# Performance work log

Measured on AMD Instinct MI355X. Metric: run time of the kernel, lower is better.

The kernel has to match this reference:

```python
import jax, jax.numpy as jnp
import numpy as np

NB, CIN, COUT, MID, G, K = 16, 128, 256, 128, 8, 64
GP = MID // G  # group_planes = 16
EPS = 1e-5


def _bn(x, g, b, axes):
    # train-mode batchnorm (biased var), channel axis = 1
    m = jnp.mean(x, axes, keepdims=True)
    v = jnp.var(x, axes, keepdims=True)
    sh = (1, -1) + (1,) * (x.ndim - 2)
    return g.reshape(sh) * (x - m) * jax.lax.rsqrt(v + EPS) + b.reshape(sh)


def _axial(x, qkv_w, bq_g, bq_b, bs_g, bs_b, bo_g, bo_b, rel):
    # x: [B, MID, K]; attention along last axis
    B = x.shape[0]
    qkv = _bn(jnp.einsum('oc,bcl->bol', qkv_w, x), bq_g, bq_b, (0, 2))
    qkv = qkv.reshape(B, G, 2 * GP, K)
    q, k, v = qkv[:, :, :GP // 2], qkv[:, :, GP // 2:GP], qkv[:, :, GP:]
    # relative position embedding lookup: rel [2*GP, 2K-1]
    idx = jnp.arange(K)[:, None] - jnp.arange(K)[None, :] + K - 1  # [K,K]
    emb = rel[:, idx]  # [2*GP, K, K]
    q_e, k_e, v_e = emb[:GP // 2], emb[GP // 2:GP], emb[GP:]
    qr = 0.1 * jnp.einsum('bgci,cij->bgij', q, q_e)          # f_qr = 0.1
    kr = 0.1 * jnp.einsum('bgci,cij->bgji', k, k_e)          # f_kr, transpose fused
    qk = jnp.einsum('bgci,bgcj->bgij', q, k)
    sim = jnp.concatenate([qk, qr, kr], axis=1)              # [B, 3G, K, K]
    sim = _bn(sim, bs_g, bs_b, (0, 2, 3)).reshape(B, 3, G, K, K).sum(1)
    sim = jax.nn.softmax(sim, axis=-1)                       # [B, G, K, K]
    sv = jnp.einsum('bgij,bgcj->bgci', sim, v)               # f_sv = 1.0
    sve = 0.1 * jnp.einsum('bgij,cij->bgci', sim, v_e)       # f_sve = 0.1
    out = jnp.concatenate([sv, sve], axis=1).reshape(B, 2 * MID, K)
    out = _bn(out, bo_g, bo_b, (0, 2))
    return out.reshape(B, MID, 2, K).sum(2)                  # [B, MID, K]


def _block(x, c1_w, c1_b, cd_w, cd_b, bn1_g, bn1_b,
           h_qkv_w, h_bq_g, h_bq_b, h_bs_g, h_bs_b, h_bo_g, h_bo_b, h_rel,
           w_qkv_w, w_bq_g, w_bq_b, w_bs_g, w_bs_b, w_bo_g, w_bo_b, w_rel,
           cu_w, cu_b, bn2_g, bn2_b):
    x_out = jnp.einsum('oc,nchw->nohw', c1_w, x) + c1_b[None, :, None, None]
    out = jnp.einsum('oc,nchw->nohw', cd_w, x) + cd_b[None, :, None, None]
    out = jax.nn.relu(_bn(out, bn1_g, bn1_b, (0, 2, 3)))
    N = out.shape[0]
    # height block: x.permute(0,3,1,2) -> [N, W, C, H] -> [N*W, C, H]
    h_in = out.transpose(0, 3, 1, 2).reshape(N * K, MID, K)
    h = _axial(h_in, h_qkv_w, h_bq_g, h_bq_b, h_bs_g, h_bs_b, h_bo_g, h_bo_b, h_rel)
    h = h.reshape(N, K, MID, K).transpose(0, 2, 3, 1)  # [N, C, H, W]
    # width block: x.permute(0,2,1,3) -> [N, H, C, W] -> [N*H, C, W]
    w_in = h.transpose(0, 2, 1, 3).reshape(N * K, MID, K)
    w = _axial(w_in, w_qkv_w, w_bq_g, w_bq_b, w_bs_g, w_bs_b, w_bo_g, w_bo_b, w_rel)
    w = w.reshape(N, K, MID, K).transpose(0, 2, 1, 3)  # [N, C, H, W]
    out = jnp.einsum('oc,nchw->nohw', cu_w, w) + cu_b[None, :, None, None]
    out = _bn(out, bn2_g, bn2_b, (0, 2, 3))
    return out + x_out


def setup_inputs() -> dict:
    key = jax.random.key(0)
    ks = jax.random.split(key, 12)
    d = {}
    d['x'] = jax.random.normal(ks[0], (NB, CIN, K, K), jnp.float32)
    d['c1_w'] = jax.random.normal(ks[1], (COUT, CIN), jnp.float32) * np.sqrt(1.0 / CIN)
    d['c1_b'] = jnp.zeros((COUT,), jnp.float32)
    d['cd_w'] = jax.random.normal(ks[2], (MID, CIN), jnp.float32) * np.sqrt(1.0 / CIN)
    d['cd_b'] = jnp.zeros((MID,), jnp.float32)
    d['bn1_g'] = jnp.ones((MID,), jnp.float32); d['bn1_b'] = jnp.zeros((MID,), jnp.float32)
    for i, p in enumerate(['h_', 'w_']):
        d[p + 'qkv_w'] = jax.random.normal(ks[3 + i], (2 * MID, MID), jnp.float32) * np.sqrt(1.0 / MID)
        d[p + 'bq_g'] = jnp.ones((2 * MID,), jnp.float32); d[p + 'bq_b'] = jnp.zeros((2 * MID,), jnp.float32)
        d[p + 'bs_g'] = jnp.ones((3 * G,), jnp.float32); d[p + 'bs_b'] = jnp.zeros((3 * G,), jnp.float32)
        d[p + 'bo_g'] = jnp.ones((2 * MID,), jnp.float32); d[p + 'bo_b'] = jnp.zeros((2 * MID,), jnp.float32)
        d[p + 'rel'] = jax.random.normal(ks[5 + i], (2 * GP, 2 * K - 1), jnp.float32) * np.sqrt(1.0 / GP)
    d['cu_w'] = jax.random.normal(ks[7], (COUT, MID), jnp.float32) * np.sqrt(1.0 / MID)
    d['cu_b'] = jnp.zeros((COUT,), jnp.float32)
    d['bn2_g'] = jnp.ones((COUT,), jnp.float32); d['bn2_b'] = jnp.zeros((COUT,), jnp.float32)
    return d


def reference(x, c1_w, c1_b, cd_w, cd_b, bn1_g, bn1_b,
              h_qkv_w, h_bq_g, h_bq_b, h_bs_g, h_bs_b, h_bo_g, h_bo_b, h_rel,
              w_qkv_w, w_bq_g, w_bq_b, w_bs_g, w_bs_b, w_bo_g, w_bo_b, w_rel,
              cu_w, cu_b, bn2_g, bn2_b):
    return _block(x, c1_w, c1_b, cd_w, cd_b, bn1_g, bn1_b,
                  h_qkv_w, h_bq_g, h_bq_b, h_bs_g, h_bs_b, h_bo_g, h_bo_b, h_rel,
                  w_qkv_w, w_bq_g, w_bq_b, w_bs_g, w_bs_b, w_bo_g, w_bo_b, w_rel,
                  cu_w, cu_b, bn2_g, bn2_b)
```

## Files before the change

### kernel.cpp

```cpp
#include <hip/hip_runtime.h>


#define NCOPY 64

typedef __attribute__((ext_vector_type(8))) short bf16x8;
typedef __attribute__((ext_vector_type(4))) short bf16x4;
typedef __attribute__((ext_vector_type(4))) float f32x4;
typedef __attribute__((ext_vector_type(2))) float f32x2;

__device__ __forceinline__ float wave_sum(float v){
  #pragma unroll
  for (int o = 32; o; o >>= 1) v += __shfl_xor(v, o, 64);
  return v;
}
__device__ __forceinline__ ushort f2bf(float f){
  union { float f; unsigned u; } v; v.f = f;
  unsigned r = v.u + 0x7FFFu + ((v.u >> 16) & 1u);
  return (ushort)(r >> 16);
}
__device__ __forceinline__ float bf2f(ushort u){
  union { unsigned u; float f; } v; v.u = ((unsigned)u) << 16;
  return v.f;
}

__global__ void k_cvt5(const float* __restrict__ s0, const float* __restrict__ s1,
                       const float* __restrict__ s2, const float* __restrict__ s3,
                       const float* __restrict__ s4, ushort* __restrict__ dst){
  int i = blockIdx.x*256 + threadIdx.x;
  if (i >= 147456) return;
  float v;
  if      (i < 16384)  v = s0[i];
  else if (i < 49152)  v = s1[i-16384];
  else if (i < 81920)  v = s2[i-49152];
  else if (i < 114688) v = s3[i-81920];
  else                 v = s4[i-114688];
  dst[i] = f2bf(v);
}

template<int O, int MODE, int SLOG, int INBF, int OUTBF>
__global__ __launch_bounds__(256) void k_gemm(
    const void* __restrict__ X_, const ushort* __restrict__ Wb,
    const float* __restrict__ bias, void* __restrict__ out_,
    float* __restrict__ acc, const ushort* __restrict__ y2,
    const float* __restrict__ scsh, ushort* __restrict__ vout)
{
  constexpr int RPW = O/4;
  constexpr int NS  = RPW/16;
  __shared__ ushort XT[64*128];

  const int tid = threadIdx.x;
  const int col0 = blockIdx.x << 6;
  const int seg  = col0 >> SLOG;
  const int p0   = col0 & ((1<<SLOG)-1);

  {
    const int col = tid & 63;
    const int kc8 = tid >> 6;
    #pragma unroll
    for (int q = 0; q < 4; ++q){
      int kc = kc8*4 + q;
      int c0 = kc*8;
      bf16x8 pk;
      if constexpr (INBF){
        const ushort* xb = (const ushort*)X_ + (((size_t)seg*128) << SLOG) + p0 + col;
        #pragma unroll
        for (int j = 0; j < 8; ++j)
          pk[j] = (short)xb[(size_t)(c0+j) << SLOG];
      } else {
        const float* xb = (const float*)X_ + (((size_t)seg*128) << SLOG) + p0 + col;
        #pragma unroll
        for (int j = 0; j < 8; ++j)
          pk[j] = (short)f2bf(xb[(size_t)(c0+j) << SLOG]);
      }
      *(bf16x8*)&XT[col*128 + ((kc ^ (col & 15)) << 3)] = pk;
    }
  }
  __syncthreads();

  const int lane = tid & 63;
  const int wid  = tid >> 6;
  const int l15  = lane & 15, lg = lane >> 4;

  f32x4 accr[NS][4];
  #pragma unroll
  for (int s = 0; s < NS; ++s)
    #pragma unroll
    for (int ns = 0; ns < 4; ++ns)
      accr[s][ns] = (f32x4){0.f,0.f,0.f,0.f};

  #pragma unroll
  for (int kk = 0; kk < 4; ++kk){
    bf16x8 af[NS];
    #pragma unroll
    for (int s = 0; s < NS; ++s){
      int m = wid*RPW + s*16 + l15;
      af[s] = *(const bf16x8*)(Wb + (size_t)m*128 + kk*32 + lg*8);
    }
    bf16x8 bfr[4];
    #pragma unroll
    for (int ns = 0; ns < 4; ++ns){
      int ncol  = ns*16 + l15;
      int chunk = kk*4 + lg;
      bfr[ns] = *(const bf16x8*)&XT[ncol*128 + ((chunk ^ l15) << 3)];
    }
    #pragma unroll
    for (int s = 0; s < NS; ++s)
      #pragma unroll
      for (int ns = 0; ns < 4; ++ns)
        accr[s][ns] = __builtin_amdgcn_mfma_f32_16x16x32_bf16(
                        af[s], bfr[ns], accr[s][ns], 0, 0, 0);
  }

  float* accb = (MODE != 2) ? acc + (size_t)(blockIdx.x & (NCOPY-1))*2*O : nullptr;
  #pragma unroll
  for (int s = 0; s < NS; ++s){
    #pragma unroll
    for (int r = 0; r < 4; ++r){
      const int m = wid*RPW + s*16 + lg*4 + r;
      const float bs = (MODE == 0 || MODE == 2) ? bias[m] : 0.f;
      float vsum = 0.f, vsq = 0.f;
      #pragma unroll
      for (int ns = 0; ns < 4; ++ns){
        float v = accr[s][ns][r] + bs;
        if constexpr (MODE == 3){
          const int cm = ((m >> 5) << 4) + (m & 15);
          size_t oidx = (((size_t)seg*128 + cm) << SLOG) + p0 + ns*16 + l15;
          if ((s & 1) == 0) ((float*)out_)[oidx] = v;
          else              vout[oidx] = f2bf(v);
        } else {
          size_t oidx = (((size_t)seg*O + m) << SLOG) + p0 + ns*16 + l15;
          if (MODE == 2)
            v += fmaf(scsh[m], bf2f(y2[oidx]), scsh[O+m]);
          if constexpr (OUTBF) ((ushort*)out_)[oidx] = f2bf(v);
          else                 ((float*) out_)[oidx] = v;
        }
        vsum += v; vsq = fmaf(v, v, vsq);
      }
      if (MODE != 2){
        #pragma unroll
        for (int o2 = 1; o2 < 16; o2 <<= 1){
          vsum += __shfl_xor(vsum, o2, 64);
          vsq  += __shfl_xor(vsq , o2, 64);
        }
        if (l15 == 0){
          atomicAdd(&accb[m],   vsum);
          atomicAdd(&accb[O+m], vsq);
        }
      }
    }
  }
}

__global__ void k_finalize(const float* __restrict__ acc, const float* __restrict__ g,
    const float* __restrict__ b, float* __restrict__ scsh, int C, float invcnt)
{
  int c = blockIdx.x*blockDim.x + threadIdx.x;
  if (c >= C) return;
  float s = 0.f, s2 = 0.f;
  #pragma unroll 4
  for (int k2 = 0; k2 < NCOPY; ++k2){
    s  += acc[(size_t)k2*2*C + c];
    s2 += acc[(size_t)k2*2*C + C + c];
  }
  float mean = s*invcnt;
  float var  = s2*invcnt - mean*mean;
  float sc = g[c]*rsqrtf(var + 1e-5f);
  scsh[c]   = sc;
  scsh[C+c] = fmaf(-mean, sc, b[c]);
}

__global__ __launch_bounds__(256) void k_trans_bnrelu(const ushort* __restrict__ out0,
    const float* __restrict__ scsh, ushort* __restrict__ hin)
{
  __shared__ float t[64][66];
  const int c = blockIdx.x, n = blockIdx.y;
  const int tid = threadIdx.x;
  const float sc = scsh[c], sh = scsh[128+c];
  const uint* src = (const uint*)(out0 + ((size_t)n*128 + c)*4096);
  #pragma unroll
  for (int r = 0; r < 8; ++r){
    int u = tid + r*256;
    uint a = src[u];
    f32x2 vv; vv.x = bf2f((ushort)a); vv.y = bf2f((ushort)(a >> 16));
    *(f32x2*)&t[u >> 5][(u & 31)*2] = vv;
  }
  __syncthreads();
  uint* dst = (uint*)(hin + (size_t)(n*64)*8192 + (size_t)c*64);
  #pragma unroll
  for (int r = 0; r < 8; ++r){
    int u = tid + r*256;
    int w = u >> 5, hp = u & 31;
    float v0 = fmaxf(fmaf(sc, t[2*hp    ][w], sh), 0.f);
    float v1 = fmaxf(fmaf(sc, t[2*hp + 1][w], sh), 0.f);
    dst[(size_t)w*4096 + hp] = ((uint)f2bf(v1) << 16) | f2bf(v0);
  }
}

__global__ __launch_bounds__(256) void k_prep_rel2(const float* __restrict__ relh,
    const float* __restrict__ relw, float* __restrict__ rwh, float* __restrict__ rww)
{
  const float* rel = (blockIdx.x & 2) ? relw : relh;
  float* rw        = (blockIdx.x & 2) ? rww  : rwh;
  const int side = blockIdx.x & 1;
  const float* base = rel + side*8*127;
  float* Wout = rw + side*4096;
  float* Sout = rw + 8192 + side*512;
  const int tid = threadIdx.y*64 + threadIdx.x;
  for (int idx = tid; idx < 4096; idx += 256){
    int pr = idx >> 6, i = idx & 63;
    int c = pr >> 3, c2 = pr & 7;
    const float* r1 = base + c*127 + i;
    const float* r2 = base + c2*127 + i;
    float s = 0.f;
    #pragma unroll 8
    for (int u = 0; u < 64; ++u) s = fmaf(r1[u], r2[u], s);
    Wout[idx] = s;
  }
  for (int idx = tid; idx < 512; idx += 256){
    int c = idx >> 6, i = idx & 63;
    const float* r1 = base + c*127 + i;
    float s = 0.f;
    #pragma unroll 8
    for (int u = 0; u < 64; ++u) s += r1[u];
    Sout[idx] = s;
  }
}

__global__ __launch_bounds__(256, 4) void k_att_stats(const float* __restrict__ qk32,
    const float* __restrict__ bq, const float* __restrict__ rw, float* __restrict__ accsim)
{
  __shared__ float WqS[4096], WkS[4096], SqS[512], SkS[512];
  const int b = blockIdx.x;
  const int tx = threadIdx.x, ty = threadIdx.y;
  const int tid = ty*64 + tx;
  for (int idx = tid; idx < 4096; idx += 256){ WqS[idx] = rw[idx]; WkS[idx] = rw[4096+idx]; }
  for (int idx = tid; idx < 512;  idx += 256){ SqS[idx] = rw[8192+idx]; SkS[idx] = rw[8704+idx]; }
  __syncthreads();
  float* accb = accsim + (size_t)(b & (NCOPY-1)) * 48;
  const int i = tx;
  const int l15 = tx & 15, lg = tx >> 4;
  const short one_bf = (short)0x3F80;
  const bf16x8 ones = {one_bf,one_bf,one_bf,one_bf,one_bf,one_bf,one_bf,one_bf};

  #pragma unroll
  for (int gi = 0; gi < 2; ++gi){
    const int g = ty*2 + gi;
    float q[8], k[8];
    #pragma unroll
    for (int c = 0; c < 8; ++c){
      int oq = g*32 + c, ok = oq + 8;
      q[c] = fmaf(bq[oq], qk32[((size_t)b*128 + g*16 + c    )*64 + i], bq[256+oq]);
      k[c] = fmaf(bq[ok], qk32[((size_t)b*128 + g*16 + 8 + c)*64 + i], bq[256+ok]);
    }
    const int och = g*32 + l15;
    const float gsc = bq[och], gsh = bq[256+och];
    const float* src = &qk32[((size_t)b*128 + g*16 + l15)*64 + lg*8];
    bf16x8 a0, a1;
    #pragma unroll
    for (int j = 0; j < 8; ++j) a0[j] = (short)f2bf(fmaf(gsc, src[j],      gsh));
    #pragma unroll
    for (int j = 0; j < 8; ++j) a1[j] = (short)f2bf(fmaf(gsc, src[32 + j], gsh));
    f32x4 G = (f32x4){0.f,0.f,0.f,0.f};
    f32x4 R = (f32x4){0.f,0.f,0.f,0.f};
    G = __builtin_amdgcn_mfma_f32_16x16x32_bf16(a0, a0, G, 0, 0, 0);
    G = __builtin_amdgcn_mfma_f32_16x16x32_bf16(a1, a1, G, 0, 0, 0);
    R = __builtin_amdgcn_mfma_f32_16x16x32_bf16(a0, ones, R, 0, 0, 0);
    R = __builtin_amdgcn_mfma_f32_16x16x32_bf16(a1, ones, R, 0, 0, 0);
    float ss = 0.f, sqk = 0.f;
    const bool gq_lane = (l15 < 8) && (lg < 2);
    const bool r_lane  = (l15 == 0) && (lg < 2);
    #pragma unroll
    for (int r = 0; r < 4; ++r){
      float gsw = __shfl_xor(G[r], 40, 64);
      float rsw = __shfl_xor(R[r], 32, 64);
      if (gq_lane) ss  = fmaf(G[r], gsw, ss);
      if (r_lane)  sqk = fmaf(R[r], rsw, sqk);
    }
    float aq = 0.f, ak = 0.f, aq2 = 0.f, ak2 = 0.f;
    #pragma unroll
    for (int c = 0; c < 8; ++c){
      aq = fmaf(q[c], SqS[c*64 + i], aq);
      ak = fmaf(k[c], SkS[c*64 + i], ak);
    }
    #pragma unroll
    for (int c = 0; c < 8; ++c){
      #pragma unroll
      for (int c2 = c; c2 < 8; ++c2){
        float w2 = (c2 == c) ? 1.f : 2.f;
        aq2 = fmaf(w2*q[c]*q[c2], WqS[(c*8+c2)*64 + i], aq2);
        ak2 = fmaf(w2*k[c]*k[c2], WkS[(c*8+c2)*64 + i], ak2);
      }
    }
    sqk = wave_sum(sqk);  ss  = wave_sum(ss);
    aq  = wave_sum(aq);   ak  = wave_sum(ak);
    aq2 = wave_sum(aq2);  ak2 = wave_sum(ak2);
    if (tx == 0){
      atomicAdd(&accb[g],      sqk);       atomicAdd(&accb[24+g],    ss);
      atomicAdd(&accb[8+g],    0.1f*aq);   atomicAdd(&accb[24+8+g],  0.01f*aq2);
      atomicAdd(&accb[16+g],   0.1f*ak);   atomicAdd(&accb[24+16+g], 0.01f*ak2);
    }
  }
}

__global__ __launch_bounds__(256) void k_att2(const float* __restrict__ qk32,
    const ushort* __restrict__ vbf, const float* __restrict__ bq,
    const float* __restrict__ rel, const float* __restrict__ simsc,
    ushort* __restrict__ svout, float* __restrict__ accbo)
{
  __shared__ __align__(16) char smem[32768];
  float* REQT = (float*)(smem);
  float* REKT = (float*)(smem + 6144);
  float* KT   = (float*)(smem + 12288);
  float* MP   = (float*)(smem + 30720);
  float* SP   = (float*)(smem + 31744);
  float* RINV = (float*)(smem + 30720);

  const int b = blockIdx.x, g = blockIdx.y;
  const int tx = threadIdx.x, ty = threadIdx.y;
  const int tid = ty*64 + tx;
  const float scq  = simsc[g];
  const float scr_ = 0.1f*simsc[8+g];
  const float sck_ = 0.1f*simsc[16+g];

  if (tid < 128){
    int j = tid & 63, h = tid >> 6;
    f32x4 kv;
    #pragma unroll
    for (int e = 0; e < 4; ++e){
      int o = g*32 + 8 + h*4 + e;
      kv[e] = fmaf(bq[o], qk32[((size_t)b*128 + g*16 + 8 + h*4 + e)*64 + j], bq[256+o]);
    }
    *(f32x4*)(KT + j*8 + h*4) = kv;
  }
  if (tid < 254){
    int side = tid >= 127;
    int d = tid - side*127;
    float rs = side ? sck_ : scr_;
    float* dst = (side ? REKT : REQT) + d*12;
    f32x4 r0, r1;
    #pragma unroll
    for (int e = 0; e < 4; ++e) r0[e] = rel[(side*8 + e)*127 + d]*rs;
    #pragma unroll
    for (int e = 0; e < 4; ++e) r1[e] = rel[(side*8 + 4 + e)*127 + d]*rs;
    *(f32x4*)dst = r0; *(f32x4*)(dst+4) = r1;
  }
  {
    int c = tid >> 4, j4 = (tid & 15)*4;
    int o = g*32 + 16 + c;
    float gsc = bq[o], gsh = bq[256+o];
    const ushort* src = &vbf[((size_t)b*128 + g*16 + c)*64 + j4];
    bf16x4 pv;
    #pragma unroll
    for (int e = 0; e < 4; ++e) pv[e] = (short)f2bf(fmaf(gsc, bf2f(src[e]), gsh));
    *(bf16x4*)(smem + 24576 + c*128 + (((j4>>3) ^ (c&7))<<4) + (j4&7)*2) = pv;
  }
  {
    int c = tid >> 4, d8 = (tid & 15)*8;
    const float* rsrc = &rel[(16+c)*127 + d8];
    bf16x8 pk;
    #pragma unroll
    for (int e = 0; e < 8; ++e){
      int d = d8 + e;
      pk[e] = (d < 127) ? (short)f2bf(0.1f*rsrc[e]) : (short)0;
    }
    *(bf16x8*)(smem + 26624 + c*256 + (((d8>>3) ^ (c&15))<<4)) = pk;
  }
  float q8[8], qs8[8];
  #pragma unroll
  for (int c = 0; c < 8; ++c){
    int o = g*32 + c;
    float qv = fmaf(bq[o], qk32[((size_t)b*128 + g*16 + c)*64 + tx], bq[256+o]);
    q8[c] = qv; qs8[c] = scq*qv;
  }
  __syncthreads();

  float acc[16];
  {
    const int j0 = ty*16;
    const f32x2* q2  = (const f32x2*)q8;
    const f32x2* qs2 = (const f32x2*)qs8;
    #pragma unroll
    for (int t = 0; t < 16; ++t){
      const int j = j0 + t;
      const f32x2* kt = (const f32x2*)(KT + j*8);
      const f32x2* rq = (const f32x2*)(REQT + (tx - j + 63)*12);
      const f32x2* rk = (const f32x2*)(REKT + (j - tx + 63)*12);
      f32x2 a2 = (f32x2){0.f, 0.f};
      #pragma unroll
      for (int c2 = 0; c2 < 4; ++c2){
        f32x2 ktv = kt[c2];
        a2 = __builtin_elementwise_fma(qs2[c2], ktv,    a2);
        a2 = __builtin_elementwise_fma(q2[c2],  rq[c2], a2);
        a2 = __builtin_elementwise_fma(ktv,     rk[c2], a2);
      }
      acc[t] = a2.x + a2.y;
    }
  }
  {
    float m0 = fmaxf(fmaxf(acc[0],acc[1]),  fmaxf(acc[2],acc[3]));
    float m1 = fmaxf(fmaxf(acc[4],acc[5]),  fmaxf(acc[6],acc[7]));
    float m2 = fmaxf(fmaxf(acc[8],acc[9]),  fmaxf(acc[10],acc[11]));
    float m3 = fmaxf(fmaxf(acc[12],acc[13]),fmaxf(acc[14],acc[15]));
    MP[ty*64 + tx] = fmaxf(fmaxf(m0,m1), fmaxf(m2,m3));
  }
  __syncthreads();

  {
    f32x4 z = (f32x4){0.f,0.f,0.f,0.f};
    float* zp = (float*)(smem + 8192 + tid*64);
    *(f32x4*)(zp+0) = z; *(f32x4*)(zp+4) = z;
    *(f32x4*)(zp+8) = z; *(f32x4*)(zp+12) = z;
  }
  {
    float mrow = fmaxf(fmaxf(MP[tx], MP[64+tx]), fmaxf(MP[128+tx], MP[192+tx]));
    float s = 0.f;
    #pragma unroll
    for (int t = 0; t < 16; ++t){ float ex = __expf(acc[t]-mrow); acc[t] = ex; s += ex; }
    SP[ty*64 + tx] = s;
  }
  __syncthreads();

  if (ty == 0)
    RINV[tx] = 1.0f / ((SP[tx] + SP[64+tx]) + (SP[128+tx] + SP[192+tx]));
  {
    bf16x8 pk0, pk1;
    #pragma unroll
    for (int e = 0; e < 8; ++e){ pk0[e] = (short)f2bf(acc[e]); pk1[e] = (short)f2bf(acc[8+e]); }
    char* pbbase = smem + 0 + tx*128;
    *(bf16x8*)(pbbase + (((2*ty    ) ^ (tx&7))<<4)) = pk0;
    *(bf16x8*)(pbbase + (((2*ty + 1) ^ (tx&7))<<4)) = pk1;
    char* ppbase = smem + 8192 + tx*256;
    #pragma unroll
    for (int e = 0; e < 16; ++e){
      int j = ty*16 + e, d = tx - j + 63;
      *(ushort*)(ppbase + (((d>>3) ^ (tx&15))<<4) + (d&7)*2) = f2bf(acc[e]);
    }
  }
  __syncthreads();

  {
    const int l15 = tx & 15, lg = tx >> 4;
    const int i0 = ty*16;
    const int rowA = i0 + l15;
    char* pbA = smem + 0    + rowA*128;
    char* ppA = smem + 8192 + rowA*256;
    char* vbB = smem + 24576 + l15*128;
    char* reB = smem + 26624 + l15*256;
    f32x4 accv = (f32x4){0.f,0.f,0.f,0.f};
    f32x4 acce = (f32x4){0.f,0.f,0.f,0.f};
    #pragma unroll
    for (int kk = 0; kk < 2; ++kk){
      bf16x8 a  = *(bf16x8*)(pbA + (((kk*4+lg) ^ (rowA&7))<<4));
      bf16x8 bb = *(bf16x8*)(vbB + (((kk*4+lg) ^ (l15&7))<<4));
      accv = __builtin_amdgcn_mfma_f32_16x16x32_bf16(a, bb, accv, 0, 0, 0);
    }
    #pragma unroll
    for (int kk = 0; kk < 4; ++kk){
      bf16x8 a  = *(bf16x8*)(ppA + (((kk*4+lg) ^ (rowA&15))<<4));
      bf16x8 bb = *(bf16x8*)(reB + (((kk*4+lg) ^ (l15&15))<<4));
      acce = __builtin_amdgcn_mfma_f32_16x16x32_bf16(a, bb, acce, 0, 0, 0);
    }
    f32x4 ri4 = *(f32x4*)(smem + 30720 + (i0 + lg*4)*4);
    float* accb = accbo + (size_t)(b & (NCOPY-1)) * 512;
    {
      bf16x4 vb4;
      float vsum = 0.f, vsq = 0.f;
      #pragma unroll
      for (int r = 0; r < 4; ++r){
        float v = accv[r]*ri4[r];
        vb4[r] = (short)f2bf(v); vsum += v; vsq = fmaf(v, v, vsq);
      }
      int ch = g*16 + l15;
      *(bf16x4*)&svout[((size_t)b*256 + ch)*64 + i0 + lg*4] = vb4;
      vsum += __shfl_xor(vsum, 16, 64); vsum += __shfl_xor(vsum, 32, 64);
      vsq  += __shfl_xor(vsq , 16, 64); vsq  += __shfl_xor(vsq , 32, 64);
      if (lg == 0){ atomicAdd(&accb[ch], vsum); atomicAdd(&accb[256+ch], vsq); }
    }
    {
      bf16x4 vb4;
      float vsum = 0.f, vsq = 0.f;
      #pragma unroll
      for (int r = 0; r < 4; ++r){
        float v = acce[r]*ri4[r];
        vb4[r] = (short)f2bf(v); vsum += v; vsq = fmaf(v, v, vsq);
      }
      int ch = 128 + g*16 + l15;
      *(bf16x4*)&svout[((size_t)b*256 + ch)*64 + i0 + lg*4] = vb4;
      vsum += __shfl_xor(vsum, 16, 64); vsum += __shfl_xor(vsum, 32, 64);
      vsq  += __shfl_xor(vsq , 16, 64); vsq  += __shfl_xor(vsq , 32, 64);
      if (lg == 0){ atomicAdd(&accb[ch], vsum); atomicAdd(&accb[256+ch], vsq); }
    }
  }
}

__global__ __launch_bounds__(256) void k_pairT(const ushort* __restrict__ sv,
    const float* __restrict__ bo, ushort* __restrict__ win)
{
  __shared__ float t[64][66];
  const int c = blockIdx.x, n = blockIdx.y;
  const int tid = threadIdx.x;
  const float s0 = bo[2*c], s1 = bo[2*c+1];
  const float sh = bo[256 + 2*c] + bo[256 + 2*c + 1];
  const ushort* base = sv + (size_t)(n*64)*256*64;
  #pragma unroll
  for (int r = 0; r < 8; ++r){
    int u = tid + r*256;
    int w = u >> 5, hp = u & 31;
    uint a = *(const uint*)&base[((size_t)w*256 + 2*c    )*64 + 2*hp];
    uint bwd = *(const uint*)&base[((size_t)w*256 + 2*c + 1)*64 + 2*hp];
    float a0 = bf2f((ushort)a),   a1 = bf2f((ushort)(a >> 16));
    float b0 = bf2f((ushort)bwd), b1 = bf2f((ushort)(bwd >> 16));
    f32x2 vv;
    vv.x = fmaf(s0, a0, fmaf(s1, b0, sh));
    vv.y = fmaf(s0, a1, fmaf(s1, b1, sh));
    *(f32x2*)&t[w][2*hp] = vv;
  }
  __syncthreads();
  uint* dst = (uint*)(win + (size_t)(n*64)*8192 + (size_t)c*64);
  #pragma unroll
  for (int r = 0; r < 8; ++r){
    int u = tid + r*256;
    int h = u >> 5, wp = u & 31;
    float v0 = t[2*wp    ][h];
    float v1 = t[2*wp + 1][h];
    dst[(size_t)h*4096 + wp] = ((uint)f2bf(v1) << 16) | f2bf(v0);
  }
}

__global__ __launch_bounds__(256) void k_pair_w(const ushort* __restrict__ sv,
    const float* __restrict__ bo, ushort* __restrict__ wbuf)
{
  const int m = blockIdx.x, n = blockIdx.y;
  const int tid = threadIdx.x;
  const float s0 = bo[2*m], s1 = bo[2*m+1];
  const float sh = bo[256 + 2*m] + bo[256 + 2*m + 1];
  const uint* p0 = (const uint*)(sv + ((size_t)(n*64)*256 + 2*m    )*64);
  const uint* p1 = (const uint*)(sv + ((size_t)(n*64)*256 + 2*m + 1)*64);
  uint* dst = (uint*)(wbuf + ((size_t)(n*128 + m)*64)*64);
  #pragma unroll
  for (int r = 0; r < 8; ++r){
    int u = tid + r*256;
    int h = u >> 5, wp = u & 31;
    uint a = p0[(size_t)h*8192 + wp];
    uint bwd = p1[(size_t)h*8192 + wp];
    float a0 = bf2f((ushort)a),   a1 = bf2f((ushort)(a >> 16));
    float b0 = bf2f((ushort)bwd), b1 = bf2f((ushort)(bwd >> 16));
    float r0 = fmaf(s0, a0, fmaf(s1, b0, sh));
    float r1 = fmaf(s0, a1, fmaf(s1, b1, sh));
    dst[(size_t)u] = ((uint)f2bf(r1) << 16) | f2bf(r0);
  }
}


extern "C" void kernel_launch(void* const* d_in, const int* in_sizes, int n_in,
                              void* d_out, int out_size, void* d_ws, size_t ws_size,
                              hipStream_t stream)
{
  const float* x     = (const float*)d_in[0];
  const float* c1_w  = (const float*)d_in[1];
  const float* c1_b  = (const float*)d_in[2];
  const float* cd_w  = (const float*)d_in[3];
  const float* cd_b  = (const float*)d_in[4];
  const float* bn1_g = (const float*)d_in[5];
  const float* bn1_b = (const float*)d_in[6];
  const float* h_qkv = (const float*)d_in[7];
  const float* h_bqg = (const float*)d_in[8];
  const float* h_bqb = (const float*)d_in[9];
  const float* h_bsg = (const float*)d_in[10];
  const float* h_bsb = (const float*)d_in[11];
  const float* h_bog = (const float*)d_in[12];
  const float* h_bob = (const float*)d_in[13];
  const float* h_rel = (const float*)d_in[14];
  const float* w_qkv = (const float*)d_in[15];
  const float* w_bqg = (const float*)d_in[16];
  const float* w_bqb = (const float*)d_in[17];
  const float* w_bsg = (const float*)d_in[18];
  const float* w_bsb = (const float*)d_in[19];
  const float* w_bog = (const float*)d_in[20];
  const float* w_bob = (const float*)d_in[21];
  const float* w_rel = (const float*)d_in[22];
  const float* cu_w  = (const float*)d_in[23];
  const float* cu_b  = (const float*)d_in[24];
  const float* bn2_g = (const float*)d_in[25];
  const float* bn2_b = (const float*)d_in[26];
  float* out = (float*)d_out;
  char* ws = (char*)d_ws;

  ushort* OUT0  = (ushort*)(ws + 0);
  ushort* HIN   = (ushort*)(ws + (32ull<<20));
  float*  QK32H = (float*)(ws + (64ull<<20));
  ushort* VBFH  = (ushort*)(ws + (96ull<<20));
  ushort* SVO   = (ushort*)(ws + 0);
  ushort* WIN   = (ushort*)(ws + (64ull<<20));
  float*  QK32W = (float*)(ws + (96ull<<20));
  ushort* VBFW  = (ushort*)(ws + (128ull<<20));
  ushort* WBUF  = (ushort*)(ws + (64ull<<20));
  ushort* Y2    = (ushort*)(ws + (96ull<<20));
  float*  ST    = (float*)(ws + (160ull<<20));

  float* ACC_BN1 = ST;
  float* ACC_BQ  = ST + 16384;
  float* ACC_SIM = ST + 49152;
  float* ACC_BO  = ST + 52224;
  float* ACC_BQW = ST + 84992;
  float* ACC_SIMW= ST + 117760;
  float* ACC_BOW = ST + 120832;
  float* ACC_BN2 = ST + 153600;
  float* SCB     = ST + 186368;
  float* SC_BN1 = SCB;        float* SC_BQ  = SCB + 256;
  float* SC_SIM = SCB + 768;  float* SC_BO  = SCB + 816;
  float* SC_BQW = SCB + 1328; float* SC_SIMW= SCB + 1840;
  float* SC_BOW = SCB + 1888; float* SC_BN2 = SCB + 2400;
  float* RWH  = ST + 189280;
  float* RWW  = ST + 198496;
  ushort* CDBF = (ushort*)(ST + 207712);
  ushort* QHBF = CDBF + 16384;
  ushort* QWBF = CDBF + 49152;
  ushort* CUBF = CDBF + 81920;
  ushort* C1BF = CDBF + 114688;

  hipMemsetAsync(ST, 0, 186368*sizeof(float), stream);

  const dim3 blk(64,4);
  const float inv64k = 1.f/65536.f;
  const float invsim = 1.f/4194304.f;

  k_cvt5<<<576, 256, 0, stream>>>(cd_w, h_qkv, w_qkv, cu_w, c1_w, CDBF);
  k_prep_rel2<<<4, blk, 0, stream>>>(h_rel, w_rel, RWH, RWW);

  k_gemm<128,0,12,0,1><<<1024, 256, 0, stream>>>(x, CDBF, cd_b, OUT0, ACC_BN1, nullptr, nullptr, nullptr);
  k_finalize<<<1, 128, 0, stream>>>(ACC_BN1, bn1_g, bn1_b, SC_BN1, 128, inv64k);
  k_trans_bnrelu<<<dim3(128,16), 256, 0, stream>>>(OUT0, SC_BN1, HIN);

  k_gemm<256,3,6,1,0><<<1024, 256, 0, stream>>>(HIN, QHBF, nullptr, QK32H, ACC_BQ, nullptr, nullptr, VBFH);
  k_finalize<<<1, 256, 0, stream>>>(ACC_BQ, h_bqg, h_bqb, SC_BQ, 256, inv64k);
  k_att_stats<<<1024, blk, 0, stream>>>(QK32H, SC_BQ, RWH, ACC_SIM);
  k_finalize<<<1, 32, 0, stream>>>(ACC_SIM, h_bsg, h_bsb, SC_SIM, 24, invsim);
  k_att2<<<dim3(1024,8), blk, 0, stream>>>(QK32H, VBFH, SC_BQ, h_rel, SC_SIM, SVO, ACC_BO);
  k_finalize<<<1, 256, 0, stream>>>(ACC_BO, h_bog, h_bob, SC_BO, 256, inv64k);
  k_pairT<<<dim3(128,16), 256, 0, stream>>>(SVO, SC_BO, WIN);

  k_gemm<256,3,6,1,0><<<1024, 256, 0, stream>>>(WIN, QWBF, nullptr, QK32W, ACC_BQW, nullptr, nullptr, VBFW);
  k_finalize<<<1, 256, 0, stream>>>(ACC_BQW, w_bqg, w_bqb, SC_BQW, 256, inv64k);
  k_att_stats<<<1024, blk, 0, stream>>>(QK32W, SC_BQW, RWW, ACC_SIMW);
  k_finalize<<<1, 32, 0, stream>>>(ACC_SIMW, w_bsg, w_bsb, SC_SIMW, 24, invsim);
  k_att2<<<dim3(1024,8), blk, 0, stream>>>(QK32W, VBFW, SC_BQW, w_rel, SC_SIMW, SVO, ACC_BOW);
  k_finalize<<<1, 256, 0, stream>>>(ACC_BOW, w_bog, w_bob, SC_BOW, 256, inv64k);
  k_pair_w<<<dim3(128,16), 256, 0, stream>>>(SVO, SC_BOW, WBUF);

  k_gemm<256,0,12,1,1><<<1024, 256, 0, stream>>>(WBUF, CUBF, cu_b, Y2, ACC_BN2, nullptr, nullptr, nullptr);
  k_finalize<<<1, 256, 0, stream>>>(ACC_BN2, bn2_g, bn2_b, SC_BN2, 256, inv64k);
  k_gemm<256,2,12,0,0><<<1024, 256, 0, stream>>>(x, C1BF, c1_b, out, nullptr, Y2, SC_BN2, nullptr);
}
```

Baseline: 375.6 us.

## Merge prep kernels, store triangular rel-pair table, pair two rows in att2 logits

Fuses the weight-conversion and relative-embedding prep kernels into one launch. The pairwise rel product table now holds only the upper-triangular 36 channel pairs instead of 64, which shrinks the att_stats shared-memory footprint so the launch bound can rise from 4 to 7 blocks per CU. The att2 logit loop now handles two key positions per iteration, loading KT with wider vector reads and keeping separate accumulators. The aim is fewer launches, higher occupancy and more instruction-level parallelism, in exchange for extra register pressure and some index arithmetic.

```diff
diff --git a/kernel.cpp b/kernel.cpp
--- a/kernel.cpp
+++ b/kernel.cpp
@@ -23,18 +23,53 @@
   return v.f;
 }
 
-__global__ void k_cvt5(const float* __restrict__ s0, const float* __restrict__ s1,
-                       const float* __restrict__ s2, const float* __restrict__ s3,
-                       const float* __restrict__ s4, ushort* __restrict__ dst){
-  int i = blockIdx.x*256 + threadIdx.x;
-  if (i >= 147456) return;
-  float v;
-  if      (i < 16384)  v = s0[i];
-  else if (i < 49152)  v = s1[i-16384];
-  else if (i < 81920)  v = s2[i-49152];
-  else if (i < 114688) v = s3[i-81920];
-  else                 v = s4[i-114688];
-  dst[i] = f2bf(v);
+__global__ void k_pre(const float* __restrict__ s0, const float* __restrict__ s1,
+                      const float* __restrict__ s2, const float* __restrict__ s3,
+                      const float* __restrict__ s4, ushort* __restrict__ dst,
+                      const float* __restrict__ relh, const float* __restrict__ relw,
+                      float* __restrict__ rwh, float* __restrict__ rww){
+  const int blk = blockIdx.x;
+  if (blk < 576){
+    int i = blk*256 + threadIdx.x;
+    if (i >= 147456) return;
+    float v;
+    if      (i < 16384)  v = s0[i];
+    else if (i < 49152)  v = s1[i-16384];
+    else if (i < 81920)  v = s2[i-49152];
+    else if (i < 114688) v = s3[i-81920];
+    else                 v = s4[i-114688];
+    dst[i] = f2bf(v);
+  } else {
+    const int sidx = blk - 576;
+    const float* rel = (sidx & 2) ? relw : relh;
+    float* rw        = (sidx & 2) ? rww  : rwh;
+    const int side = sidx & 1;
+    const float* base = rel + side*8*127;
+    float* Wout = rw + side*2304;
+    float* Sout = rw + 4608 + side*512;
+    const int tid = threadIdx.x;
+    for (int idx = tid; idx < 2304; idx += 256){
+      int pr = idx >> 6, i = idx & 63;
+      int c = 0, off = pr;
+      #pragma unroll
+      for (int cc = 0; cc < 7; ++cc){ if (off >= 8 - c){ off -= (8 - c); ++c; } }
+      int c2 = c + off;
+      const float* r1 = base + c*127 + i;
+      const float* r2 = base + c2*127 + i;
+      float s = 0.f;
+      #pragma unroll 8
+      for (int u = 0; u < 64; ++u) s = fmaf(r1[u], r2[u], s);
+      Wout[idx] = s;
+    }
+    for (int idx = tid; idx < 512; idx += 256){
+      int c = idx >> 6, i = idx & 63;
+      const float* r1 = base + c*127 + i;
+      float s = 0.f;
+      #pragma unroll 8
+      for (int u = 0; u < 64; ++u) s += r1[u];
+      Sout[idx] = s;
+    }
+  }
 }
 
 template<int O, int MODE, int SLOG, int INBF, int OUTBF>
@@ -196,51 +231,22 @@
   }
 }
 
-__global__ __launch_bounds__(256) void k_prep_rel2(const float* __restrict__ relh,
-    const float* __restrict__ relw, float* __restrict__ rwh, float* __restrict__ rww)
-{
-  const float* rel = (blockIdx.x & 2) ? relw : relh;
-  float* rw        = (blockIdx.x & 2) ? rww  : rwh;
-  const int side = blockIdx.x & 1;
-  const float* base = rel + side*8*127;
-  float* Wout = rw + side*4096;
-  float* Sout = rw + 8192 + side*512;
-  const int tid = threadIdx.y*64 + threadIdx.x;
-  for (int idx = tid; idx < 4096; idx += 256){
-    int pr = idx >> 6, i = idx & 63;
-    int c = pr >> 3, c2 = pr & 7;
-    const float* r1 = base + c*127 + i;
-    const float* r2 = base + c2*127 + i;
-    float s = 0.f;
-    #pragma unroll 8
-    for (int u = 0; u < 64; ++u) s = fmaf(r1[u], r2[u], s);
-    Wout[idx] = s;
-  }
-  for (int idx = tid; idx < 512; idx += 256){
-    int c = idx >> 6, i = idx & 63;
-    const float* r1 = base + c*127 + i;
-    float s = 0.f;
-    #pragma unroll 8
-    for (int u = 0; u < 64; ++u) s += r1[u];
-    Sout[idx] = s;
-  }
-}
-
-__global__ __launch_bounds__(256, 4) void k_att_stats(const float* __restrict__ qk32,
+__global__ __launch_bounds__(256, 7) void k_att_stats(const float* __restrict__ qk32,
     const float* __restrict__ bq, const float* __restrict__ rw, float* __restrict__ accsim)
 {
-  __shared__ float WqS[4096], WkS[4096], SqS[512], SkS[512];
+  __shared__ float WqS[2304], WkS[2304], SqS[512], SkS[512];
   const int b = blockIdx.x;
   const int tx = threadIdx.x, ty = threadIdx.y;
   const int tid = ty*64 + tx;
-  for (int idx = tid; idx < 4096; idx += 256){ WqS[idx] = rw[idx]; WkS[idx] = rw[4096+idx]; }
-  for (int idx = tid; idx < 512;  idx += 256){ SqS[idx] = rw[8192+idx]; SkS[idx] = rw[8704+idx]; }
+  for (int idx = tid; idx < 2304; idx += 256){ WqS[idx] = rw[idx]; WkS[idx] = rw[2304+idx]; }
+  for (int idx = tid; idx < 512;  idx += 256){ SqS[idx] = rw[4608+idx]; SkS[idx] = rw[5120+idx]; }
   __syncthreads();
   float* accb = accsim + (size_t)(b & (NCOPY-1)) * 48;
   const int i = tx;
   const int l15 = tx & 15, lg = tx >> 4;
   const short one_bf = (short)0x3F80;
   const bf16x8 ones = {one_bf,one_bf,one_bf,one_bf,one_bf,one_bf,one_bf,one_bf};
+  constexpr int tb[8] = {0,8,15,21,26,30,33,35};
 
   #pragma unroll
   for (int gi = 0; gi < 2; ++gi){
@@ -287,8 +293,9 @@
       #pragma unroll
       for (int c2 = c; c2 < 8; ++c2){
         float w2 = (c2 == c) ? 1.f : 2.f;
-        aq2 = fmaf(w2*q[c]*q[c2], WqS[(c*8+c2)*64 + i], aq2);
-        ak2 = fmaf(w2*k[c]*k[c2], WkS[(c*8+c2)*64 + i], ak2);
+        int pi = (tb[c] + c2 - c)*64 + i;
+        aq2 = fmaf(w2*q[c]*q[c2], WqS[pi], aq2);
+        ak2 = fmaf(w2*k[c]*k[c2], WkS[pi], ak2);
       }
     }
     sqk = wave_sum(sqk);  ss  = wave_sum(ss);
@@ -380,20 +387,33 @@
     const f32x2* q2  = (const f32x2*)q8;
     const f32x2* qs2 = (const f32x2*)qs8;
     #pragma unroll
-    for (int t = 0; t < 16; ++t){
-      const int j = j0 + t;
-      const f32x2* kt = (const f32x2*)(KT + j*8);
-      const f32x2* rq = (const f32x2*)(REQT + (tx - j + 63)*12);
-      const f32x2* rk = (const f32x2*)(REKT + (j - tx + 63)*12);
-      f32x2 a2 = (f32x2){0.f, 0.f};
+    for (int p = 0; p < 8; ++p){
+      const int j = j0 + 2*p;
+      float kbuf[16];
+      *(f32x4*)(kbuf+0)  = *(const f32x4*)(KT + j*8 + 0);
+      *(f32x4*)(kbuf+4)  = *(const f32x4*)(KT + j*8 + 4);
+      *(f32x4*)(kbuf+8)  = *(const f32x4*)(KT + j*8 + 8);
+      *(f32x4*)(kbuf+12) = *(const f32x4*)(KT + j*8 + 12);
+      const f32x2* ktA = (const f32x2*)(kbuf);
+      const f32x2* ktB = (const f32x2*)(kbuf + 8);
+      const f32x2* rqA = (const f32x2*)(REQT + (tx - j + 63)*12);
+      const f32x2* rqB = (const f32x2*)(REQT + (tx - j + 62)*12);
+      const f32x2* rkA = (const f32x2*)(REKT + (j - tx + 63)*12);
+      const f32x2* rkB = (const f32x2*)(REKT + (j - tx + 64)*12);
+      f32x2 aA = (f32x2){0.f,0.f}, bA = (f32x2){0.f,0.f};
+      f32x2 aB = (f32x2){0.f,0.f}, bB = (f32x2){0.f,0.f};
       #pragma unroll
       for (int c2 = 0; c2 < 4; ++c2){
-        f32x2 ktv = kt[c2];
-        a2 = __builtin_elementwise_fma(qs2[c2], ktv,    a2);
-        a2 = __builtin_elementwise_fma(q2[c2],  rq[c2], a2);
-        a2 = __builtin_elementwise_fma(ktv,     rk[c2], a2);
+        f32x2 kvA = ktA[c2], kvB = ktB[c2];
+        aA = __builtin_elementwise_fma(qs2[c2], kvA,     aA);
+        aA = __builtin_elementwise_fma(q2[c2],  rqA[c2], aA);
+        bA = __builtin_elementwise_fma(kvA,     rkA[c2], bA);
+        aB = __builtin_elementwise_fma(qs2[c2], kvB,     aB);
+        aB = __builtin_elementwise_fma(q2[c2],  rqB[c2], aB);
+        bB = __builtin_elementwise_fma(kvB,     rkB[c2], bB);
       }
-      acc[t] = a2.x + a2.y;
+      acc[2*p]     = (aA.x + aA.y) + (bA.x + bA.y);
+      acc[2*p + 1] = (aB.x + aB.y) + (bB.x + bB.y);
     }
   }
   {
@@ -625,8 +645,8 @@
   const float inv64k = 1.f/65536.f;
   const float invsim = 1.f/4194304.f;
 
-  k_cvt5<<<576, 256, 0, stream>>>(cd_w, h_qkv, w_qkv, cu_w, c1_w, CDBF);
-  k_prep_rel2<<<4, blk, 0, stream>>>(h_rel, w_rel, RWH, RWW);
+  k_pre<<<580, 256, 0, stream>>>(cd_w, h_qkv, w_qkv, cu_w, c1_w, CDBF,
+                                 h_rel, w_rel, RWH, RWW);
 
   k_gemm<128,0,12,0,1><<<1024, 256, 0, stream>>>(x, CDBF, cd_b, OUT0, ACC_BN1, nullptr, nullptr, nullptr);
   k_finalize<<<1, 128, 0, stream>>>(ACC_BN1, bn1_g, bn1_b, SC_BN1, 128, inv64k);
```

Measured after the change: 376.2 us. No clear change (+0.2%).
